# Optimization experiments

Measured on AMD Instinct MI355X. Metric: run time of the kernel, lower is better.

The kernel has to match this reference:

```python
import jax, jax.numpy as jnp
import numpy as np

N, G = 50000, 2500
PER = N // G                 # 20 nodes per graph
M, Z, NB, WIDTH, K = 128, 4, 8, 128, 3
INV = 3 * M                  # 384 invariant features
COV = 9 * M                  # 1152 = 128*(1+3+5)
GAMMA = 10.0
D_MIN, D_MAX = 0.9, 1.8
D_CENTER, D_HALF = 0.5 * (D_MIN + D_MAX), 0.5 * (D_MAX - D_MIN)
SQ_MZ = float(np.sqrt(M * Z))  # e3nn path normalization (fan_in = mul1*mul2)
P_GRID = 4096                # Fibonacci sphere quadrature for SO3 normalizer

_i = np.arange(P_GRID)
_ph = np.pi * (3.0 - np.sqrt(5.0)) * _i
_z = 1.0 - 2.0 * (_i + 0.5) / P_GRID
_r = np.sqrt(np.maximum(1.0 - _z * _z, 0.0))
FIB = np.stack([_r * np.cos(_ph), _r * np.sin(_ph), _z], 1).astype(np.float32)

def real_sh(v):
    # real spherical harmonics up to l=2, integral normalization, m=-l..l
    x, y, z = v[..., 0], v[..., 1], v[..., 2]
    c0, c1 = 0.28209479177387814, 0.4886025119029199
    ca, c20, c22 = 1.0925484305920792, 0.31539156525252005, 0.5462742152960396
    return jnp.stack([c0 * jnp.ones_like(x), c1 * y, c1 * z, c1 * x,
                      ca * x * y, ca * y * z, c20 * (3 * z * z - 1.0),
                      ca * x * z, c22 * (x * x - y * y)], -1)

Y_GRID = np.asarray(real_sh(jnp.asarray(FIB)))  # [P_GRID, 9]

def split_cov(x):
    lead = x.shape[:-1]
    return (x[..., :M].reshape(*lead, M, 1),
            x[..., M:4 * M].reshape(*lead, M, 3),
            x[..., 4 * M:9 * M].reshape(*lead, M, 5))

def setup_inputs():
    key = jax.random.key(0)
    ks = jax.random.split(key, 16)
    s_inter = jax.random.normal(ks[0], (N, COV), jnp.float32)
    bag = jnp.floor(jax.random.uniform(ks[1], (G, Z)) * 5.0).at[:, 0].add(1.0)
    batch = jnp.repeat(jnp.arange(G, dtype=jnp.int32), PER)
    ptr = jnp.arange(G + 1, dtype=jnp.int32) * PER
    focus = jax.random.randint(ks[2], (G,), 0, PER, jnp.int32)
    element = jnp.zeros((G,), jnp.int32)  # column 0 of bag is always > 0
    distance = D_MIN + (D_MAX - D_MIN) * jax.random.uniform(ks[3], (G,), jnp.float32)
    ori = jax.random.normal(ks[4], (G, 3), jnp.float32)
    orientation = ori / jnp.linalg.norm(ori, axis=-1, keepdims=True)
    W_bag = jax.random.normal(ks[5], (3, M, Z, M), jnp.float32)
    def lin(k, i, o):
        return jax.random.normal(k, (i, o), jnp.float32) / np.sqrt(i).astype(np.float32)
    return dict(
        s_inter=s_inter, bag=bag, batch=batch, ptr=ptr, focus=focus,
        element=element, distance=distance, orientation=orientation,
        W_bag=W_bag,
        d_log_stds=jnp.full((K,), np.log(0.1), jnp.float32),
        W_mix=jax.random.normal(ks[6], (NB, 3 * M * Z), jnp.float32),
        W1f=lin(ks[7], INV, WIDTH), b1f=jnp.zeros(WIDTH), W2f=lin(ks[8], WIDTH, 1), b2f=jnp.zeros(1),
        W1e=lin(ks[9], INV, WIDTH), b1e=jnp.zeros(WIDTH), W2e=lin(ks[10], WIDTH, Z), b2e=jnp.zeros(Z),
        W1d=lin(ks[11], INV + Z, WIDTH), b1d=jnp.zeros(WIDTH), W2d=lin(ks[12], WIDTH, 2 * K), b2d=jnp.zeros(2 * K),
    )

def reference(s_inter, bag, batch, ptr, focus, element, distance, orientation,
              W_bag, d_log_stds, W_mix,
              W1f, b1f, W2f, b2f, W1e, b1e, W2e, b2e, W1d, b1d, W2d, b2d):
    bag_n = bag[batch]                                  # [N, Z]
    xs = split_cov(s_inter)
    covs = [jnp.einsum('nim,nz,izo->nom', xs[l], bag_n, W_bag[l]) / SQ_MZ for l in range(3)]
    s_cov = jnp.concatenate([c.reshape(N, -1) for c in covs], -1)   # [N, 1152]
    s_inv = jnp.concatenate([jnp.sqrt(jnp.sum(c * c, -1) + 1e-12) for c in covs], -1)  # [N, 384]
    # --- focus: per-graph scatter softmax over nodes ---
    fl = (jax.nn.relu(s_inv @ W1f + b1f) @ W2f + b2f)[:, 0]
    mx = jax.ops.segment_max(fl, batch, num_segments=G)
    ex = jnp.exp(fl - mx[batch])
    focus_probs = ex / jax.ops.segment_sum(ex, batch, num_segments=G)[batch]
    gidx = focus + ptr[:-1]
    lp_focus = jnp.log(focus_probs[gidx] + 1e-20)
    # --- element: bag-masked softmax ---
    el = jax.nn.relu(s_inv @ W1e + b1e) @ W2e + b2e
    mask = (bag > 0)[batch]
    all_element_probs = jax.nn.softmax(jnp.where(mask, el, -1e9), -1)
    foc_el = all_element_probs[gidx]
    lp_element = jnp.log(jnp.take_along_axis(foc_el, element[:, None], 1)[:, 0] + 1e-20)
    element_oh = jax.nn.one_hot(element, Z, dtype=s_inter.dtype)
    # --- distance: Gaussian mixture head ---
    d_in = jnp.concatenate([s_inv[gidx], element_oh], -1)
    h = jax.nn.relu(d_in @ W1d + b1d) @ W2d + b2d
    gmm_logits, d_mean_t = h[:, :K], h[:, K:]
    d_mean = jnp.tanh(d_mean_t) * D_HALF + D_CENTER
    stds = jnp.maximum(jnp.exp(d_log_stds), 1e-6)
    logw = jax.nn.log_softmax(gmm_logits, -1)
    comp = -0.5 * ((distance[:, None] - d_mean) / stds) ** 2 - jnp.log(stds) - 0.5 * np.log(2 * np.pi).astype(np.float32)
    lp_dist = jax.nn.logsumexp(logw + comp, -1)
    # --- mix tensor product with bessel-conditioned external weights ---
    kk = jnp.arange(1, NB + 1, dtype=s_inter.dtype)
    bess = np.sqrt(2.0 / D_MAX).astype(np.float32) * jnp.sin(kk * np.pi * distance[:, None] / D_MAX) / distance[:, None]
    tpw = ((bess @ W_mix) / np.sqrt(NB).astype(np.float32)).reshape(G, 3, M, Z)
    foc = split_cov(s_cov[gidx])
    cond = [jnp.einsum('gim,gz,giz->gm', foc[l], element_oh, tpw[:, l]) / SQ_MZ for l in range(3)]
    cond_cov = jnp.concatenate(cond, -1)                # [G, 9]
    # --- SO(3) distribution: p(x) ~ exp(gamma * <a, Y(x)>), normalized on sphere grid ---
    ori = orientation / jnp.linalg.norm(orientation, axis=-1, keepdims=True)
    f_x = jnp.sum(cond_cov * real_sh(ori), -1)
    f_grid = cond_cov @ jnp.asarray(Y_GRID).T           # [G, P_GRID]
    logZ = jax.nn.logsumexp(GAMMA * f_grid, -1) - np.log(P_GRID).astype(np.float32) + np.log(4 * np.pi).astype(np.float32)
    lp_ori = GAMMA * f_x - logZ
    logp = lp_focus + lp_element + lp_dist + lp_ori
    # --- entropies: focus entropy + element|focus conditional entropy ---
    h_focus = -jax.ops.segment_sum(focus_probs * jnp.log(focus_probs + 1e-20), batch, num_segments=G)
    h_el = -jnp.sum(all_element_probs * jnp.log(jnp.maximum(all_element_probs, 1e-20)), -1)
    h_ef = jax.ops.segment_sum(focus_probs * h_el, batch, num_segments=G)
    entropy = h_focus + h_ef
    return jnp.stack([logp, entropy], -1)               # [G, 2]
```

## Files before the change

### kernel.cpp

```cpp
#include <hip/hip_runtime.h>
#include <math.h>

#define NN 50000
#define GG 2500
#define WS_YG    0
#define WS_SINV  36864
#define WS_FL    (WS_SINV + 19200000)
#define WS_HEL   (WS_FL + 50000)
#define WS_LPEL  (WS_HEL + 50000)
#define WS_SCOV  (WS_LPEL + 50000)
#define WS_TOTAL (WS_SCOV + 2880000)

__device__ __forceinline__ void real_sh9(float x, float y, float z, float* o) {
  const float c0 = 0.28209479177387814f;
  const float c1 = 0.4886025119029199f;
  const float ca = 1.0925484305920792f;
  const float c20 = 0.31539156525252005f;
  const float c22 = 0.5462742152960396f;
  o[0] = c0;
  o[1] = c1 * y;
  o[2] = c1 * z;
  o[3] = c1 * x;
  o[4] = ca * x * y;
  o[5] = ca * y * z;
  o[6] = c20 * (3.f * z * z - 1.f);
  o[7] = ca * x * z;
  o[8] = c22 * (x * x - y * y);
}

__global__ void k_ygrid(float* __restrict__ yg) {
  int i = blockIdx.x * blockDim.x + threadIdx.x;
  if (i >= 4096) return;
  double fr = 0.38196601125010515 * (double)i;
  fr -= floor(fr);
  float ph = (float)(fr * 6.283185307179586);
  float z = 1.0f - 2.0f * ((float)i + 0.5f) * (1.0f / 4096.0f);
  float r = sqrtf(fmaxf(1.f - z * z, 0.f));
  float x = r * cosf(ph);
  float y = r * sinf(ph);
  float sh[9];
  real_sh9(x, y, z, sh);
#pragma unroll
  for (int m = 0; m < 9; ++m) yg[i * 9 + m] = sh[m];
}

#define FMA4(c, a, s)            \
  c.x = fmaf(a.x, s, c.x);       \
  c.y = fmaf(a.y, s, c.y);       \
  c.z = fmaf(a.z, s, c.z);       \
  c.w = fmaf(a.w, s, c.w);

#define EPI_M(ACC, M)                                                       \
  {                                                                         \
    const float e0 = ACC.x * invs, e1 = ACC.y * invs, e2 = ACC.z * invs,    \
                e3 = ACC.w * invs;                                          \
    sj0 += e0 * e0; sj1 += e1 * e1; sj2 += e2 * e2; sj3 += e3 * e3;         \
    if (isf) {                                                              \
      float* sp = scov + (size_t)g * 1152 + OFF +                           \
                  (size_t)(obase + o4) * COMP + (M);                        \
      sp[0 * COMP] = e0; sp[1 * COMP] = e1;                                 \
      sp[2 * COMP] = e2; sp[3 * COMP] = e3;                                 \
    }                                                                       \
  }

template <int L, int COMP, int OFF>
__device__ __forceinline__ void cov_block(
    const float* __restrict__ s_inter, const float* __restrict__ Wl,
    float b0, float b1, float b2, float b3,
    int n0, int nseg, int gi, int g, int obase,
    float* __restrict__ sinv, float* __restrict__ scov, float* A) {
  const int t = threadIdx.x;
  __syncthreads();
  for (int idx4 = t; idx4 < 2048; idx4 += 320) {
    const int i = idx4 >> 4, ol4 = (idx4 & 15) << 2;
    const float* wp = Wl + i * 512 + obase + ol4;
    const float4 w0 = *(const float4*)(wp);
    const float4 w1 = *(const float4*)(wp + 128);
    const float4 w2 = *(const float4*)(wp + 256);
    const float4 w3 = *(const float4*)(wp + 384);
    float4 a;
    a.x = b0 * w0.x + b1 * w1.x + b2 * w2.x + b3 * w3.x;
    a.y = b0 * w0.y + b1 * w1.y + b2 * w2.y + b3 * w3.y;
    a.z = b0 * w0.z + b1 * w1.z + b2 * w2.z + b3 * w3.z;
    a.w = b0 * w0.w + b1 * w1.w + b2 * w2.w + b3 * w3.w;
    *(float4*)(A + i * 64 + ol4) = a;
  }
  __syncthreads();
  const int o4 = (t & 15) << 2;
  const int slot = t >> 4;
  if (slot < nseg) {
    const int n = n0 + slot;
    const float* xp = s_inter + (size_t)n * 1152 + OFF;
    float4 ac0 = {0.f, 0.f, 0.f, 0.f};
    float4 ac1 = {0.f, 0.f, 0.f, 0.f};
    float4 ac2 = {0.f, 0.f, 0.f, 0.f};
    float4 ac3 = {0.f, 0.f, 0.f, 0.f};
    float4 ac4 = {0.f, 0.f, 0.f, 0.f};
    for (int i4 = 0; i4 < 128; i4 += 4) {
      const float* ap = A + i4 * 64 + o4;
      const float4 a0 = *(const float4*)(ap);
      const float4 a1 = *(const float4*)(ap + 64);
      const float4 a2 = *(const float4*)(ap + 128);
      const float4 a3 = *(const float4*)(ap + 192);
      if constexpr (COMP == 1) {
        const float4 x0 = *(const float4*)(xp + i4);
        FMA4(ac0, a0, x0.x);
        FMA4(ac0, a1, x0.y);
        FMA4(ac0, a2, x0.z);
        FMA4(ac0, a3, x0.w);
      } else if constexpr (COMP == 3) {
        const float* xq = xp + i4 * 3;
        const float4 x0 = *(const float4*)(xq);
        const float4 x1 = *(const float4*)(xq + 4);
        const float4 x2 = *(const float4*)(xq + 8);
        FMA4(ac0, a0, x0.x); FMA4(ac1, a0, x0.y); FMA4(ac2, a0, x0.z);
        FMA4(ac0, a1, x0.w); FMA4(ac1, a1, x1.x); FMA4(ac2, a1, x1.y);
        FMA4(ac0, a2, x1.z); FMA4(ac1, a2, x1.w); FMA4(ac2, a2, x2.x);
        FMA4(ac0, a3, x2.y); FMA4(ac1, a3, x2.z); FMA4(ac2, a3, x2.w);
      } else {
        const float* xq = xp + i4 * 5;
        const float4 x0 = *(const float4*)(xq);
        const float4 x1 = *(const float4*)(xq + 4);
        const float4 x2 = *(const float4*)(xq + 8);
        const float4 x3 = *(const float4*)(xq + 12);
        const float4 x4 = *(const float4*)(xq + 16);
        FMA4(ac0, a0, x0.x); FMA4(ac1, a0, x0.y); FMA4(ac2, a0, x0.z);
        FMA4(ac3, a0, x0.w); FMA4(ac4, a0, x1.x);
        FMA4(ac0, a1, x1.y); FMA4(ac1, a1, x1.z); FMA4(ac2, a1, x1.w);
        FMA4(ac3, a1, x2.x); FMA4(ac4, a1, x2.y);
        FMA4(ac0, a2, x2.z); FMA4(ac1, a2, x2.w); FMA4(ac2, a2, x3.x);
        FMA4(ac3, a2, x3.y); FMA4(ac4, a2, x3.z);
        FMA4(ac0, a3, x3.w); FMA4(ac1, a3, x4.x); FMA4(ac2, a3, x4.y);
        FMA4(ac3, a3, x4.z); FMA4(ac4, a3, x4.w);
      }
    }
    const bool isf = (n == gi);
    const float invs = 0.044194173824159216f;
    float sj0 = 1e-12f, sj1 = 1e-12f, sj2 = 1e-12f, sj3 = 1e-12f;
    EPI_M(ac0, 0);
    if constexpr (COMP > 1) {
      EPI_M(ac1, 1);
      EPI_M(ac2, 2);
    }
    if constexpr (COMP > 3) {
      EPI_M(ac3, 3);
      EPI_M(ac4, 4);
    }
    *(float4*)(sinv + (size_t)n * 384 + L * 128 + obase + o4) =
        make_float4(sqrtf(sj0), sqrtf(sj1), sqrtf(sj2), sqrtf(sj3));
  }
}

__global__ __launch_bounds__(320) void k_cov(
    const float* __restrict__ s_inter, const float* __restrict__ bag,
    const int* __restrict__ ptr, const int* __restrict__ focus,
    const float* __restrict__ W_bag,
    float* __restrict__ sinv, float* __restrict__ scov) {
  __shared__ __align__(16) float A[8192];
  const int g = blockIdx.x;
  const int obase = blockIdx.y * 64;
  const int n0 = ptr[g];
  const int nseg = ptr[g + 1] - n0;
  const int gi = n0 + focus[g];
  const float b0 = bag[g * 4 + 0], b1 = bag[g * 4 + 1];
  const float b2 = bag[g * 4 + 2], b3 = bag[g * 4 + 3];
  cov_block<0, 1, 0>(s_inter, W_bag, b0, b1, b2, b3, n0, nseg, gi, g, obase, sinv, scov, A);
  cov_block<1, 3, 128>(s_inter, W_bag + 65536, b0, b1, b2, b3, n0, nseg, gi, g, obase, sinv, scov, A);
  cov_block<2, 5, 512>(s_inter, W_bag + 131072, b0, b1, b2, b3, n0, nseg, gi, g, obase, sinv, scov, A);
}

__global__ __launch_bounds__(128) void k_mlp(
    const float* __restrict__ sinv, const float* __restrict__ bag,
    const int* __restrict__ batch, const int* __restrict__ element,
    const float* __restrict__ W1f, const float* __restrict__ b1f,
    const float* __restrict__ W2f, const float* __restrict__ b2f,
    const float* __restrict__ W1e, const float* __restrict__ b1e,
    const float* __restrict__ W2e, const float* __restrict__ b2e,
    float* __restrict__ flv, float* __restrict__ helv, float* __restrict__ lpelv) {
  __shared__ __align__(16) float lds[4224];
  __shared__ float els[16][4];
  const int t = threadIdx.x;
  const int n0 = blockIdx.x * 16;
  float af[16], ae[16];
#pragma unroll
  for (int p = 0; p < 16; ++p) { af[p] = 0.f; ae[p] = 0.f; }
  const float bf = b1f[t], be = b1e[t];
  for (int cb = 0; cb < 6; ++cb) {
    const int c0 = cb * 64;
    __syncthreads();
    {
      const int p = t >> 3, q = (t & 7) * 8;
      const float* src = sinv + (size_t)(n0 + p) * 384 + c0 + q;
      const float4 v0 = *(const float4*)(src);
      const float4 v1 = *(const float4*)(src + 4);
      *(float4*)(lds + p * 64 + q) = v0;
      *(float4*)(lds + p * 64 + q + 4) = v1;
    }
    __syncthreads();
    for (int cc = 0; cc < 64; cc += 4) {
      const int c = c0 + cc;
      const float wf0 = W1f[(c + 0) * 128 + t];
      const float wf1 = W1f[(c + 1) * 128 + t];
      const float wf2 = W1f[(c + 2) * 128 + t];
      const float wf3 = W1f[(c + 3) * 128 + t];
      const float we0 = W1e[(c + 0) * 128 + t];
      const float we1 = W1e[(c + 1) * 128 + t];
      const float we2 = W1e[(c + 2) * 128 + t];
      const float we3 = W1e[(c + 3) * 128 + t];
#pragma unroll
      for (int p = 0; p < 16; ++p) {
        const float4 s4 = *(const float4*)(lds + p * 64 + cc);
        af[p] = fmaf(s4.x, wf0, af[p]);
        af[p] = fmaf(s4.y, wf1, af[p]);
        af[p] = fmaf(s4.z, wf2, af[p]);
        af[p] = fmaf(s4.w, wf3, af[p]);
        ae[p] = fmaf(s4.x, we0, ae[p]);
        ae[p] = fmaf(s4.y, we1, ae[p]);
        ae[p] = fmaf(s4.z, we2, ae[p]);
        ae[p] = fmaf(s4.w, we3, ae[p]);
      }
    }
  }
  __syncthreads();
#pragma unroll
  for (int p = 0; p < 16; ++p) {
    lds[p * 132 + t] = fmaxf(af[p] + bf, 0.f);
    lds[2112 + p * 132 + t] = fmaxf(ae[p] + be, 0.f);
  }
  __syncthreads();
  if (t < 80) {
    const int p = t / 5, q = t - p * 5;
    if (q == 0) {
      float s = 0.f;
      for (int j = 0; j < 128; ++j) s = fmaf(lds[p * 132 + j], W2f[j], s);
      flv[n0 + p] = s + b2f[0];
    } else {
      const int z = q - 1;
      float s = 0.f;
      for (int j = 0; j < 128; ++j) s = fmaf(lds[2112 + p * 132 + j], W2e[j * 4 + z], s);
      els[p][z] = s + b2e[z];
    }
  }
  __syncthreads();
  if (t < 16) {
    const int n = n0 + t;
    const int g = batch[n];
    const int elem = element[g];
    float v[4];
#pragma unroll
    for (int z = 0; z < 4; ++z) {
      const bool mk = bag[g * 4 + z] > 0.f;
      v[z] = mk ? els[t][z] : -1e9f;
    }
    const float mx = fmaxf(fmaxf(v[0], v[1]), fmaxf(v[2], v[3]));
    float e[4];
    float S = 0.f;
#pragma unroll
    for (int z = 0; z < 4; ++z) { e[z] = expf(v[z] - mx); S += e[z]; }
    const float iS = 1.f / S;
    float h = 0.f;
#pragma unroll
    for (int z = 0; z < 4; ++z) {
      const float pz = e[z] * iS;
      h -= pz * logf(fmaxf(pz, 1e-20f));
    }
    helv[n] = h;
    lpelv[n] = logf(e[elem] * iS + 1e-20f);
  }
}

__global__ __launch_bounds__(128) void k_group(
    const int* __restrict__ ptr, const int* __restrict__ focus,
    const int* __restrict__ element, const float* __restrict__ distance,
    const float* __restrict__ orientation, const float* __restrict__ dls,
    const float* __restrict__ W_mix,
    const float* __restrict__ W1d, const float* __restrict__ b1d,
    const float* __restrict__ W2d, const float* __restrict__ b2d,
    const float* __restrict__ flv, const float* __restrict__ helv,
    const float* __restrict__ lpelv, const float* __restrict__ sinv,
    const float* __restrict__ scov, const float* __restrict__ yg,
    float* __restrict__ out) {
  __shared__ float fls[32];
  __shared__ float hels[32];
  __shared__ __align__(16) float svg[384];
  __shared__ float hd[128];
  __shared__ float out6[6];
  __shared__ float red[128][12];
  __shared__ float conds[9];
  __shared__ float mred[128];
  __shared__ float sred[128];
  const int g = blockIdx.x;
  const int t = threadIdx.x;
  const int n0 = ptr[g];
  const int nseg = ptr[g + 1] - n0;
  const int floc = focus[g];
  const int gi = n0 + floc;
  const int elem = element[g];
  const float dist = distance[g];
  if (t < nseg) { fls[t] = flv[n0 + t]; hels[t] = helv[n0 + t]; }
  for (int c = t; c < 384; c += 128) svg[c] = sinv[(size_t)gi * 384 + c];
  __syncthreads();
  float res_lpf = 0.f, res_ent = 0.f;
  if (t == 0) {
    float mx = -1e30f;
    for (int p = 0; p < nseg; ++p) mx = fmaxf(mx, fls[p]);
    float S = 0.f;
    for (int p = 0; p < nseg; ++p) S += expf(fls[p] - mx);
    const float iS = 1.f / S;
    float hfoc = 0.f, hef = 0.f;
    for (int p = 0; p < nseg; ++p) {
      const float pp = expf(fls[p] - mx) * iS;
      hfoc -= pp * logf(pp + 1e-20f);
      hef += pp * hels[p];
    }
    res_lpf = logf(expf(fls[floc] - mx) * iS + 1e-20f);
    res_ent = hfoc + hef;
  }
  {
    float acc = b1d[t];
    for (int c = 0; c < 384; c += 4) {
      const float4 s4 = *(const float4*)(&svg[c]);
      acc = fmaf(s4.x, W1d[(c + 0) * 128 + t], acc);
      acc = fmaf(s4.y, W1d[(c + 1) * 128 + t], acc);
      acc = fmaf(s4.z, W1d[(c + 2) * 128 + t], acc);
      acc = fmaf(s4.w, W1d[(c + 3) * 128 + t], acc);
    }
    acc += W1d[(384 + elem) * 128 + t];
    hd[t] = fmaxf(acc, 0.f);
  }
  __syncthreads();
  if (t < 6) {
    float s = 0.f;
    for (int j = 0; j < 128; ++j) s = fmaf(hd[j], W2d[j * 6 + t], s);
    out6[t] = s + b2d[t];
  }
  {
    float bess[8];
    const float sq2d = 1.0540925533894598f;
#pragma unroll
    for (int k = 0; k < 8; ++k)
      bess[k] = sq2d * sinf((float)(k + 1) * 3.14159265358979323846f * dist / 1.8f) / dist;
    const float invnb = 0.35355339059327373f;
    float partial[9];
    {
      float tw = 0.f;
#pragma unroll
      for (int k = 0; k < 8; ++k) tw += bess[k] * W_mix[k * 1536 + t * 4 + elem];
      tw *= invnb;
      partial[0] = scov[(size_t)g * 1152 + t] * tw;
    }
    {
      float tw = 0.f;
#pragma unroll
      for (int k = 0; k < 8; ++k) tw += bess[k] * W_mix[k * 1536 + (128 + t) * 4 + elem];
      tw *= invnb;
#pragma unroll
      for (int m = 0; m < 3; ++m) partial[1 + m] = scov[(size_t)g * 1152 + 128 + t * 3 + m] * tw;
    }
    {
      float tw = 0.f;
#pragma unroll
      for (int k = 0; k < 8; ++k) tw += bess[k] * W_mix[k * 1536 + (256 + t) * 4 + elem];
      tw *= invnb;
#pragma unroll
      for (int m = 0; m < 5; ++m) partial[4 + m] = scov[(size_t)g * 1152 + 512 + t * 5 + m] * tw;
    }
#pragma unroll
    for (int q = 0; q < 9; ++q) red[t][q] = partial[q];
  }
  __syncthreads();
  if (t < 9) {
    float s = 0.f;
    for (int i = 0; i < 128; ++i) s += red[i][t];
    conds[t] = s * 0.044194173824159216f;
  }
  __syncthreads();
  const float c0 = conds[0], c1 = conds[1], c2 = conds[2], c3 = conds[3];
  const float c4 = conds[4], c5 = conds[5], c6 = conds[6], c7 = conds[7];
  const float c8 = conds[8];
  float lm = -1e30f, ls = 0.f;
  for (int p = t; p < 4096; p += 128) {
    const float* yp = yg + p * 9;
    float v = c0 * yp[0] + c1 * yp[1] + c2 * yp[2] + c3 * yp[3] + c4 * yp[4] +
              c5 * yp[5] + c6 * yp[6] + c7 * yp[7] + c8 * yp[8];
    v *= 10.0f;
    if (v > lm) { ls = ls * expf(lm - v) + 1.f; lm = v; }
    else ls += expf(v - lm);
  }
  mred[t] = lm;
  sred[t] = ls;
  __syncthreads();
  if (t == 0) {
    const float l0 = out6[0], l1 = out6[1], l2 = out6[2];
    const float lmx = fmaxf(l0, fmaxf(l1, l2));
    const float lsew = lmx + logf(expf(l0 - lmx) + expf(l1 - lmx) + expf(l2 - lmx));
    float vals[3];
#pragma unroll
    for (int k = 0; k < 3; ++k) {
      const float mean = tanhf(out6[3 + k]) * 0.45f + 1.35f;
      const float sd = fmaxf(expf(dls[k]), 1e-6f);
      const float zz = (dist - mean) / sd;
      vals[k] = (out6[k] - lsew) + (-0.5f * zz * zz - logf(sd) - 0.9189385332046727f);
    }
    const float vm = fmaxf(vals[0], fmaxf(vals[1], vals[2]));
    const float lp_dist =
        vm + logf(expf(vals[0] - vm) + expf(vals[1] - vm) + expf(vals[2] - vm));
    float Mx = -1e30f;
    for (int i = 0; i < 128; ++i) Mx = fmaxf(Mx, mred[i]);
    float S = 0.f;
    for (int i = 0; i < 128; ++i) S += sred[i] * expf(mred[i] - Mx);
    const float logZ = Mx + logf(S) - 8.317766166719343f + 2.5310242469692907f;
    float ox = orientation[g * 3 + 0], oy = orientation[g * 3 + 1], oz = orientation[g * 3 + 2];
    const float inr = 1.f / sqrtf(ox * ox + oy * oy + oz * oz);
    ox *= inr; oy *= inr; oz *= inr;
    float sh[9];
    real_sh9(ox, oy, oz, sh);
    const float fx = c0 * sh[0] + c1 * sh[1] + c2 * sh[2] + c3 * sh[3] + c4 * sh[4] +
                     c5 * sh[5] + c6 * sh[6] + c7 * sh[7] + c8 * sh[8];
    const float lp_ori = 10.0f * fx - logZ;
    out[g * 2 + 0] = res_lpf + lpelv[gi] + lp_dist + lp_ori;
    out[g * 2 + 1] = res_ent;
  }
}

extern "C" void kernel_launch(void* const* d_in, const int* in_sizes, int n_in,
                              void* d_out, int out_size, void* d_ws, size_t ws_size,
                              hipStream_t stream) {
  const float* s_inter = (const float*)d_in[0];
  const float* bag = (const float*)d_in[1];
  const int* batch = (const int*)d_in[2];
  const int* ptr = (const int*)d_in[3];
  const int* focus = (const int*)d_in[4];
  const int* element = (const int*)d_in[5];
  const float* distance = (const float*)d_in[6];
  const float* orientation = (const float*)d_in[7];
  const float* W_bag = (const float*)d_in[8];
  const float* dls = (const float*)d_in[9];
  const float* W_mix = (const float*)d_in[10];
  const float* W1f = (const float*)d_in[11];
  const float* b1f = (const float*)d_in[12];
  const float* W2f = (const float*)d_in[13];
  const float* b2f = (const float*)d_in[14];
  const float* W1e = (const float*)d_in[15];
  const float* b1e = (const float*)d_in[16];
  const float* W2e = (const float*)d_in[17];
  const float* b2e = (const float*)d_in[18];
  const float* W1d = (const float*)d_in[19];
  const float* b1d = (const float*)d_in[20];
  const float* W2d = (const float*)d_in[21];
  const float* b2d = (const float*)d_in[22];

  if (ws_size < (size_t)WS_TOTAL * sizeof(float)) return;

  float* ws = (float*)d_ws;
  float* yg = ws + WS_YG;
  float* sinv = ws + WS_SINV;
  float* flv = ws + WS_FL;
  float* helv = ws + WS_HEL;
  float* lpelv = ws + WS_LPEL;
  float* scov = ws + WS_SCOV;
  float* out = (float*)d_out;

  k_ygrid<<<dim3(32), dim3(128), 0, stream>>>(yg);
  k_cov<<<dim3(GG, 2), dim3(320), 0, stream>>>(s_inter, bag, ptr, focus, W_bag, sinv, scov);
  k_mlp<<<dim3(NN / 16), dim3(128), 0, stream>>>(sinv, bag, batch, element,
                                                 W1f, b1f, W2f, b2f,
                                                 W1e, b1e, W2e, b2e,
                                                 flv, helv, lpelv);
  k_group<<<dim3(GG), dim3(128), 0, stream>>>(ptr, focus, element, distance, orientation,
                                              dls, W_mix, W1d, b1d, W2d, b2d,
                                              flv, helv, lpelv, sinv, scov, yg, out);
}
```

Before: 957.3 us.

## Merge output-column halves into one block and stage node features in LDS

The covariant projection kernel now uses one 640-thread block per graph covering all 128 output channels, instead of two 320-thread blocks each handling 64 channels. All 20 nodes' s_inter rows are first copied into shared memory, so each input row is read from global memory once per graph instead of once per column half. In exchange the block needs about 154 KB of LDS and twice as many threads, which limits how many blocks fit per CU and halves the grid size.

```diff
diff --git a/kernel.cpp b/kernel.cpp
--- a/kernel.cpp
+++ b/kernel.cpp
@@ -56,8 +56,7 @@
                 e3 = ACC.w * invs;                                          \
     sj0 += e0 * e0; sj1 += e1 * e1; sj2 += e2 * e2; sj3 += e3 * e3;         \
     if (isf) {                                                              \
-      float* sp = scov + (size_t)g * 1152 + OFF +                           \
-                  (size_t)(obase + o4) * COMP + (M);                        \
+      float* sp = scov + (size_t)g * 1152 + OFF + (size_t)o4 * COMP + (M);  \
       sp[0 * COMP] = e0; sp[1 * COMP] = e1;                                 \
       sp[2 * COMP] = e2; sp[3 * COMP] = e3;                                 \
     }                                                                       \
@@ -65,15 +64,15 @@
 
 template <int L, int COMP, int OFF>
 __device__ __forceinline__ void cov_block(
-    const float* __restrict__ s_inter, const float* __restrict__ Wl,
+    const float* __restrict__ X, const float* __restrict__ Wl,
     float b0, float b1, float b2, float b3,
-    int n0, int nseg, int gi, int g, int obase,
+    int n0, int nseg, int gi, int g,
     float* __restrict__ sinv, float* __restrict__ scov, float* A) {
   const int t = threadIdx.x;
   __syncthreads();
-  for (int idx4 = t; idx4 < 2048; idx4 += 320) {
-    const int i = idx4 >> 4, ol4 = (idx4 & 15) << 2;
-    const float* wp = Wl + i * 512 + obase + ol4;
+  for (int idx4 = t; idx4 < 4096; idx4 += 640) {
+    const int i = idx4 >> 5, ol4 = (idx4 & 31) << 2;
+    const float* wp = Wl + i * 512 + ol4;
     const float4 w0 = *(const float4*)(wp);
     const float4 w1 = *(const float4*)(wp + 128);
     const float4 w2 = *(const float4*)(wp + 256);
@@ -83,25 +82,25 @@
     a.y = b0 * w0.y + b1 * w1.y + b2 * w2.y + b3 * w3.y;
     a.z = b0 * w0.z + b1 * w1.z + b2 * w2.z + b3 * w3.z;
     a.w = b0 * w0.w + b1 * w1.w + b2 * w2.w + b3 * w3.w;
-    *(float4*)(A + i * 64 + ol4) = a;
-  }
-  __syncthreads();
-  const int o4 = (t & 15) << 2;
-  const int slot = t >> 4;
+    *(float4*)(A + i * 128 + ol4) = a;
+  }
+  __syncthreads();
+  const int o4 = (t & 31) << 2;
+  const int slot = t >> 5;
   if (slot < nseg) {
     const int n = n0 + slot;
-    const float* xp = s_inter + (size_t)n * 1152 + OFF;
+    const float* xp = X + slot * 1152 + OFF;
     float4 ac0 = {0.f, 0.f, 0.f, 0.f};
     float4 ac1 = {0.f, 0.f, 0.f, 0.f};
     float4 ac2 = {0.f, 0.f, 0.f, 0.f};
     float4 ac3 = {0.f, 0.f, 0.f, 0.f};
     float4 ac4 = {0.f, 0.f, 0.f, 0.f};
     for (int i4 = 0; i4 < 128; i4 += 4) {
-      const float* ap = A + i4 * 64 + o4;
+      const float* ap = A + i4 * 128 + o4;
       const float4 a0 = *(const float4*)(ap);
-      const float4 a1 = *(const float4*)(ap + 64);
-      const float4 a2 = *(const float4*)(ap + 128);
-      const float4 a3 = *(const float4*)(ap + 192);
+      const float4 a1 = *(const float4*)(ap + 128);
+      const float4 a2 = *(const float4*)(ap + 256);
+      const float4 a3 = *(const float4*)(ap + 384);
       if constexpr (COMP == 1) {
         const float4 x0 = *(const float4*)(xp + i4);
         FMA4(ac0, a0, x0.x);
@@ -146,27 +145,35 @@
       EPI_M(ac3, 3);
       EPI_M(ac4, 4);
     }
-    *(float4*)(sinv + (size_t)n * 384 + L * 128 + obase + o4) =
+    *(float4*)(sinv + (size_t)n * 384 + L * 128 + o4) =
         make_float4(sqrtf(sj0), sqrtf(sj1), sqrtf(sj2), sqrtf(sj3));
   }
 }
 
-__global__ __launch_bounds__(320) void k_cov(
+__global__ __launch_bounds__(640) void k_cov(
     const float* __restrict__ s_inter, const float* __restrict__ bag,
     const int* __restrict__ ptr, const int* __restrict__ focus,
     const float* __restrict__ W_bag,
     float* __restrict__ sinv, float* __restrict__ scov) {
-  __shared__ __align__(16) float A[8192];
+  __shared__ __align__(16) float A[16384];
+  __shared__ __align__(16) float X[23040];
   const int g = blockIdx.x;
-  const int obase = blockIdx.y * 64;
+  const int t = threadIdx.x;
   const int n0 = ptr[g];
   const int nseg = ptr[g + 1] - n0;
   const int gi = n0 + focus[g];
   const float b0 = bag[g * 4 + 0], b1 = bag[g * 4 + 1];
   const float b2 = bag[g * 4 + 2], b3 = bag[g * 4 + 3];
-  cov_block<0, 1, 0>(s_inter, W_bag, b0, b1, b2, b3, n0, nseg, gi, g, obase, sinv, scov, A);
-  cov_block<1, 3, 128>(s_inter, W_bag + 65536, b0, b1, b2, b3, n0, nseg, gi, g, obase, sinv, scov, A);
-  cov_block<2, 5, 512>(s_inter, W_bag + 131072, b0, b1, b2, b3, n0, nseg, gi, g, obase, sinv, scov, A);
+  for (int idx = t; idx < 5760; idx += 640) {
+    const int p = idx / 288;
+    const int q4 = (idx - p * 288) << 2;
+    if (p < nseg)
+      *(float4*)(X + p * 1152 + q4) =
+          *(const float4*)(s_inter + (size_t)(n0 + p) * 1152 + q4);
+  }
+  cov_block<0, 1, 0>(X, W_bag, b0, b1, b2, b3, n0, nseg, gi, g, sinv, scov, A);
+  cov_block<1, 3, 128>(X, W_bag + 65536, b0, b1, b2, b3, n0, nseg, gi, g, sinv, scov, A);
+  cov_block<2, 5, 512>(X, W_bag + 131072, b0, b1, b2, b3, n0, nseg, gi, g, sinv, scov, A);
 }
 
 __global__ __launch_bounds__(128) void k_mlp(
@@ -462,7 +469,7 @@
   float* out = (float*)d_out;
 
   k_ygrid<<<dim3(32), dim3(128), 0, stream>>>(yg);
-  k_cov<<<dim3(GG, 2), dim3(320), 0, stream>>>(s_inter, bag, ptr, focus, W_bag, sinv, scov);
+  k_cov<<<dim3(GG), dim3(640), 0, stream>>>(s_inter, bag, ptr, focus, W_bag, sinv, scov);
   k_mlp<<<dim3(NN / 16), dim3(128), 0, stream>>>(sinv, bag, batch, element,
                                                  W1f, b1f, W2f, b2f,
                                                  W1e, b1e, W2e, b2e,
```

After: 920.5 us. -3.8%, faster.
